# Performance work log

Hardware: AMD Instinct MI355X
Metric: run time of the kernel (lower is better)

## Reference

```python
import jax, jax.numpy as jnp
import numpy as np

N = 100000   # nodes
E = 1600000  # edges (avg degree 16)
D = 64       # input feature dim
H = 64       # hidden dim


def _uniform(k, shape, fan_in):
    s = 1.0 / np.sqrt(fan_in).astype(np.float32)
    return jax.random.uniform(k, shape, jnp.float32, -s, s)


def setup_inputs() -> dict:
    key = jax.random.key(0)
    ks = jax.random.split(key, 9)
    x = jax.random.normal(ks[0], (N, D), jnp.float32)
    edge_index = jax.random.randint(ks[1], (2, E), 0, N, dtype=jnp.int64)
    edge_weight = jax.random.uniform(ks[2], (E,), jnp.float32)
    return {
        "x": x,
        "edge_index": edge_index,
        "edge_weight": edge_weight,
        # conv1: GraphConv(D, H): lin_rel (with bias) + lin_root (no bias)
        "w1_rel": _uniform(ks[3], (H, D), D),
        "b1": _uniform(ks[4], (H,), D),
        "w1_root": _uniform(ks[5], (H, D), D),
        # conv2: GraphConv(H, H)
        "w2_rel": _uniform(ks[6], (H, H), H),
        "b2": _uniform(ks[7], (H,), H),
        "w2_root": _uniform(ks[8], (H, H), H),
    }


def _graph_conv(h, src, dst, ew, w_rel, b, w_root):
    # PyG GraphConv with aggr='add':
    #   out_i = W_rel @ sum_{(j->i) in E} ew_ji * h_j + b + W_root @ h_i
    msg = h[src] * ew[:, None]                              # [E, F] gather
    agg = jax.ops.segment_sum(msg, dst, num_segments=N)     # [N, F] scatter-add
    return agg @ w_rel.T + b + h @ w_root.T


def reference(x, edge_index, edge_weight, w1_rel, b1, w1_root, w2_rel, b2, w2_root):
    src, dst = edge_index[0], edge_index[1]
    # dropout(0.2) is identity in eval mode
    h = jax.nn.relu(_graph_conv(x, src, dst, edge_weight, w1_rel, b1, w1_root))
    h = jax.nn.relu(_graph_conv(h, src, dst, edge_weight, w2_rel, b2, w2_root))
    return h
```

## Files before the change

kernel.cpp:

```cpp
#include <hip/hip_runtime.h>
#include <cstddef>


#define FDIM 64
#define BSHC 9
#define BNC (1 << BSHC)
#define CAPC 8960

static inline size_t align256(size_t x) { return (x + 255) & ~size_t(255); }

typedef __attribute__((ext_vector_type(8))) short bf16x8;
typedef __attribute__((ext_vector_type(4))) float f32x4;

__device__ __forceinline__ ushort f2bf(float f) {
    unsigned u = __float_as_uint(f);
    unsigned r = u + 0x7fffu + ((u >> 16) & 1u);
    return (ushort)(r >> 16);
}
__device__ __forceinline__ float bflo(unsigned g) { return __uint_as_float(g << 16); }
__device__ __forceinline__ float bfhi(unsigned g) { return __uint_as_float(g & 0xffff0000u); }
__device__ __forceinline__ unsigned packbf(float lo, float hi) {
    return (unsigned)f2bf(lo) | ((unsigned)f2bf(hi) << 16);
}

__global__ void __launch_bounds__(256)
k_prep(const float* __restrict__ x, ushort* __restrict__ xb, int nflt,
       const int* __restrict__ ei, int* __restrict__ flag,
       int* __restrict__ gcur, int nbc,
       const float* __restrict__ wrel1, const float* __restrict__ wroot1,
       const float* __restrict__ wrel2, const float* __restrict__ wroot2,
       ushort* __restrict__ wp1, ushort* __restrict__ wp2) {
    int t = threadIdx.x, bid = blockIdx.x;
    int i = (bid * 256 + t) * 4;
    if (i < nflt) {
        float4 v = *reinterpret_cast<const float4*>(x + i);
        ushort4 o;
        o.x = f2bf(v.x); o.y = f2bf(v.y); o.z = f2bf(v.z); o.w = f2bf(v.w);
        *reinterpret_cast<ushort4*>(xb + i) = o;
    }
    if (bid == 0) {
        __shared__ int any;
        if (t == 0) any = 0;
        __syncthreads();
        for (int k = t; k < 2048; k += 256)
            if (ei[2 * k + 1] != 0) any = 1;
        for (int j = t; j < nbc; j += 256) gcur[j] = 0;
        __syncthreads();
        if (t == 0) *flag = (any == 0) ? 1 : 0;
    } else if (bid <= 64) {
        int tid = (bid - 1) * 256 + t;
        int layer = tid >> 13;
        int idx = tid & 8191;
        int j = idx & 7, l = (idx >> 3) & 63, og = (idx >> 9) & 3, kk = idx >> 11;
        int k = kk * 32 + ((l >> 4) << 3) + j;
        int o = og * 16 + (l & 15);
        const float* rel  = layer ? wrel2 : wrel1;
        const float* root = layer ? wroot2 : wroot1;
        float v = (k < 64) ? rel[o * FDIM + k] : root[o * FDIM + (k - 64)];
        (layer ? wp2 : wp1)[idx] = f2bf(v);
    }
}

__global__ void __launch_bounds__(512)
k_scatterC(const int* __restrict__ ei, const float* __restrict__ ew, int E,
           const int* __restrict__ flag, int* __restrict__ gcur,
           uint2* __restrict__ recs, int nbc) {
    __shared__ int hcnt[256];
    __shared__ int hbase[256];
    int t = threadIdx.x;
    int base = blockIdx.x * 4096;
    int sh = *flag;
    if (t < 256) hcnt[t] = 0;
    __syncthreads();

    int bkt[8];
    uint2 rec[8];
#pragma unroll
    for (int j = 0; j < 8; ++j) {
        int e = base + j * 512 + t;
        bkt[j] = -1;
        if (e < E) {
            int s = ei[(size_t)e << sh];
            int d = ei[(size_t)(E + e) << sh];
            bkt[j] = d >> BSHC;
            rec[j].x = (unsigned)s | ((unsigned)(d & (BNC - 1)) << 17);
            rec[j].y = __float_as_uint(ew[e]);
            atomicAdd(&hcnt[bkt[j]], 1);
        }
    }
    __syncthreads();
    if (t < nbc) {
        int c = hcnt[t];
        hbase[t] = c ? (t * CAPC + atomicAdd(&gcur[t], c)) : 0;
    }
    __syncthreads();
    if (t < 256) hcnt[t] = 0;
    __syncthreads();
#pragma unroll
    for (int j = 0; j < 8; ++j) {
        if (bkt[j] >= 0) {
            int r = atomicAdd(&hcnt[bkt[j]], 1);
            int pos = hbase[bkt[j]] + r;
            if (pos < (bkt[j] + 1) * CAPC) recs[pos] = rec[j];
        }
    }
}

__global__ void __launch_bounds__(512)
k_csrSortC(const int* __restrict__ gcur, uint2* __restrict__ recs, int n,
           int* __restrict__ rs, int* __restrict__ re) {
    __shared__ uint2 lrec[CAPC];
    __shared__ int lh[BNC];
    __shared__ int lo[BNC];
    __shared__ int lcur[BNC];
    int b = blockIdx.x, t = threadIdx.x;
    int base = b * CAPC;
    int cnt = gcur[b];
    if (cnt > CAPC) cnt = CAPC;

    for (int i = t; i < cnt; i += 512) lrec[i] = recs[base + i];
    lh[t] = 0;
    __syncthreads();
    for (int i = t; i < cnt; i += 512) atomicAdd(&lh[lrec[i].x >> 17], 1);
    __syncthreads();
    lo[t] = lh[t];
    __syncthreads();
    for (int off = 1; off < BNC; off <<= 1) {
        int v = (t >= off) ? lo[t - off] : 0;
        __syncthreads();
        lo[t] += v;
        __syncthreads();
    }
    {
        int ex = lo[t] - lh[t];
        lcur[t] = ex;
        int node = (b << BSHC) + t;
        if (node < n) { rs[node] = base + ex; re[node] = base + ex + lh[t]; }
    }
    __syncthreads();
    for (int i = t; i < cnt; i += 512) {
        uint2 r = lrec[i];
        int pos = atomicAdd(&lcur[r.x >> 17], 1);
        recs[base + pos] = make_uint2(r.x & 0x1FFFF, r.y);
    }
}

__global__ void __launch_bounds__(256)
k_aggB16(const ushort* __restrict__ hb, const int* __restrict__ rs,
         const int* __restrict__ re, const uint2* __restrict__ recs,
         int n, ushort* __restrict__ aggb) {
    int wavid = (blockIdx.x * blockDim.x + threadIdx.x) >> 6;
    int lane = threadIdx.x & 63;
    int nA = wavid << 1;
    if (nA >= n) return;
    int nB = nA + 1;
    int q = lane >> 3, sl = lane & 7;
    const uint4* hw4 = reinterpret_cast<const uint4*>(hb);
    int pA = rs[nA], eA = re[nA];
    int pB = rs[nB], eB = re[nB];

    float A0 = 0.f, A1 = 0.f, A2 = 0.f, A3 = 0.f, A4 = 0.f, A5 = 0.f, A6 = 0.f, A7 = 0.f;
    float B0 = 0.f, B1 = 0.f, B2 = 0.f, B3 = 0.f, B4 = 0.f, B5 = 0.f, B6 = 0.f, B7 = 0.f;

#define FMA8(P, g, wf)                                       \
    do {                                                     \
        float w_ = (wf);                                     \
        P##0 = fmaf(bflo((g).x), w_, P##0);                  \
        P##1 = fmaf(bfhi((g).x), w_, P##1);                  \
        P##2 = fmaf(bflo((g).y), w_, P##2);                  \
        P##3 = fmaf(bfhi((g).y), w_, P##3);                  \
        P##4 = fmaf(bflo((g).z), w_, P##4);                  \
        P##5 = fmaf(bfhi((g).z), w_, P##5);                  \
        P##6 = fmaf(bflo((g).w), w_, P##6);                  \
        P##7 = fmaf(bfhi((g).w), w_, P##7);                  \
    } while (0)

    while (pA < eA || pB < eB) {
        int iA0 = pA + q, iA1 = pA + 8 + q;
        int iB0 = pB + q, iB1 = pB + 8 + q;
        uint2 ra0 = recs[iA0];
        uint2 ra1 = recs[iA1];
        uint2 rb0 = recs[iB0];
        uint2 rb1 = recs[iB1];
        uint4 ga0 = hw4[(size_t)(ra0.x & 0x1FFFFu) * 8 + sl];
        uint4 ga1 = hw4[(size_t)(ra1.x & 0x1FFFFu) * 8 + sl];
        uint4 gb0 = hw4[(size_t)(rb0.x & 0x1FFFFu) * 8 + sl];
        uint4 gb1 = hw4[(size_t)(rb1.x & 0x1FFFFu) * 8 + sl];
        float wa0 = (iA0 < eA) ? __uint_as_float(ra0.y) : 0.f;
        float wa1 = (iA1 < eA) ? __uint_as_float(ra1.y) : 0.f;
        float wb0 = (iB0 < eB) ? __uint_as_float(rb0.y) : 0.f;
        float wb1 = (iB1 < eB) ? __uint_as_float(rb1.y) : 0.f;
        FMA8(A, ga0, wa0);
        FMA8(A, ga1, wa1);
        FMA8(B, gb0, wb0);
        FMA8(B, gb1, wb1);
        pA = (pA + 16 < eA) ? pA + 16 : eA;
        pB = (pB + 16 < eB) ? pB + 16 : eB;
    }
#undef FMA8

#define RED2(d)                                                  \
    A0 += __shfl_xor(A0, d, 64); A1 += __shfl_xor(A1, d, 64);    \
    A2 += __shfl_xor(A2, d, 64); A3 += __shfl_xor(A3, d, 64);    \
    A4 += __shfl_xor(A4, d, 64); A5 += __shfl_xor(A5, d, 64);    \
    A6 += __shfl_xor(A6, d, 64); A7 += __shfl_xor(A7, d, 64);    \
    B0 += __shfl_xor(B0, d, 64); B1 += __shfl_xor(B1, d, 64);    \
    B2 += __shfl_xor(B2, d, 64); B3 += __shfl_xor(B3, d, 64);    \
    B4 += __shfl_xor(B4, d, 64); B5 += __shfl_xor(B5, d, 64);    \
    B6 += __shfl_xor(B6, d, 64); B7 += __shfl_xor(B7, d, 64);
    RED2(8) RED2(16) RED2(32)
#undef RED2

    if (q == 0) {
        uint4 o;
        o.x = packbf(A0, A1);
        o.y = packbf(A2, A3);
        o.z = packbf(A4, A5);
        o.w = packbf(A6, A7);
        reinterpret_cast<uint4*>(aggb + (size_t)nA * FDIM)[sl] = o;
    } else if (q == 1) {
        uint4 o;
        o.x = packbf(B0, B1);
        o.y = packbf(B2, B3);
        o.z = packbf(B4, B5);
        o.w = packbf(B6, B7);
        reinterpret_cast<uint4*>(aggb + (size_t)nB * FDIM)[sl] = o;
    }
}

template<int OUTBF>
__global__ void __launch_bounds__(256)
k_denseM(const ushort* __restrict__ aggb, const ushort* __restrict__ rootb,
         const ushort* __restrict__ wp, const float* __restrict__ bias,
         float* __restrict__ outp, ushort* __restrict__ outb, int n) {
    int t = threadIdx.x;
    int wv = t >> 6, l = t & 63;
    int n0 = blockIdx.x * 64 + wv * 16;
    int row = l & 15, half = l >> 4;

    int node = n0 + row;
    bool inb = node < n;
    const ushort* ap = aggb + (size_t)node * FDIM + half * 8;
    const ushort* rp = rootb + (size_t)node * FDIM + half * 8;
    bf16x8 a0 = inb ? *reinterpret_cast<const bf16x8*>(ap)      : bf16x8{0,0,0,0,0,0,0,0};
    bf16x8 a1 = inb ? *reinterpret_cast<const bf16x8*>(ap + 32) : bf16x8{0,0,0,0,0,0,0,0};
    bf16x8 a2 = inb ? *reinterpret_cast<const bf16x8*>(rp)      : bf16x8{0,0,0,0,0,0,0,0};
    bf16x8 a3 = inb ? *reinterpret_cast<const bf16x8*>(rp + 32) : bf16x8{0,0,0,0,0,0,0,0};

    f32x4 acc[4];
#pragma unroll
    for (int og = 0; og < 4; ++og) acc[og] = f32x4{0.f, 0.f, 0.f, 0.f};

#pragma unroll
    for (int og = 0; og < 4; ++og) {
        const bf16x8* wb = reinterpret_cast<const bf16x8*>(wp) + og * 64 + l;
        acc[og] = __builtin_amdgcn_mfma_f32_16x16x32_bf16(a0, wb[0],       acc[og], 0, 0, 0);
        acc[og] = __builtin_amdgcn_mfma_f32_16x16x32_bf16(a1, wb[4 * 64],  acc[og], 0, 0, 0);
        acc[og] = __builtin_amdgcn_mfma_f32_16x16x32_bf16(a2, wb[8 * 64],  acc[og], 0, 0, 0);
        acc[og] = __builtin_amdgcn_mfma_f32_16x16x32_bf16(a3, wb[12 * 64], acc[og], 0, 0, 0);
    }

    int rbase = n0 + half * 4;
#pragma unroll
    for (int og = 0; og < 4; ++og) {
        float bb = bias[og * 16 + row];
#pragma unroll
        for (int r = 0; r < 4; ++r) {
            int nd = rbase + r;
            if (nd < n) {
                float v = fmaxf(acc[og][r] + bb, 0.f);
                if (OUTBF) outb[(size_t)nd * FDIM + og * 16 + row] = f2bf(v);
                else       outp[(size_t)nd * FDIM + og * 16 + row] = v;
            }
        }
    }
}

extern "C" void kernel_launch(void* const* d_in, const int* in_sizes, int n_in,
                              void* d_out, int out_size, void* d_ws, size_t ws_size,
                              hipStream_t stream) {
    const float* x      = (const float*)d_in[0];
    const int*   ei     = (const int*)d_in[1];
    const float* ew     = (const float*)d_in[2];
    const float* w1rel  = (const float*)d_in[3];
    const float* b1     = (const float*)d_in[4];
    const float* w1root = (const float*)d_in[5];
    const float* w2rel  = (const float*)d_in[6];
    const float* b2     = (const float*)d_in[7];
    const float* w2root = (const float*)d_in[8];
    float* out = (float*)d_out;

    int N = in_sizes[0] / FDIM;
    int E = in_sizes[2];
    int NBC = (N + BNC - 1) >> BSHC;

    char* w = (char*)d_ws;
    int* flag    = (int*)w;    w += align256(256);
    int* gcur    = (int*)w;    w += align256((size_t)NBC * 4);
    int* rs      = (int*)w;    w += align256((size_t)N * 4);
    int* re      = (int*)w;    w += align256((size_t)N * 4);
    ushort* wp1  = (ushort*)w; w += align256(8192 * 2);
    ushort* wp2  = (ushort*)w; w += align256(8192 * 2);
    uint2* recs  = (uint2*)w;  w += align256((size_t)NBC * CAPC * 8);
    ushort* aggb = (ushort*)w; w += align256((size_t)N * FDIM * 2);
    ushort* xb   = (ushort*)w; w += align256((size_t)N * FDIM * 2);
    ushort* h1b  = (ushort*)w; w += align256((size_t)N * FDIM * 2);

    int nflt = N * FDIM;
    k_prep<<<(nflt / 4 + 255) / 256, 256, 0, stream>>>(
        x, xb, nflt, ei, flag, gcur, NBC, w1rel, w1root, w2rel, w2root, wp1, wp2);
    k_scatterC<<<(E + 4095) / 4096, 512, 0, stream>>>(ei, ew, E, flag, gcur, recs, NBC);
    k_csrSortC<<<NBC, 512, 0, stream>>>(gcur, recs, N, rs, re);

    k_aggB16<<<(N + 7) / 8, 256, 0, stream>>>(xb, rs, re, recs, N, aggb);
    k_denseM<1><<<(N + 63) / 64, 256, 0, stream>>>(aggb, xb, wp1, b1, nullptr, h1b, N);
    k_aggB16<<<(N + 7) / 8, 256, 0, stream>>>(h1b, rs, re, recs, N, aggb);
    k_denseM<0><<<(N + 63) / 64, 256, 0, stream>>>(aggb, h1b, wp2, b2, out, nullptr, N);
}
```

Baseline: 140.7 us.

## Rework aggregation: half-wave per node, shuffle-broadcast edge records, adaptive gather depth

The aggregation kernel now assigns each half-wave to one node. The half-wave loads up to 32 edge records at once with one coalesced load, then broadcasts the source indices and weights through shuffles. Up to 8 gather steps are issued per iteration, limited by the remaining degree, so low-degree nodes do not fetch wasted rows. A zeroed 64-entry pad is placed after the record buffer so that reads past the end stay safe. The cross-lane reduction drops one shuffle stage, at the cost of more shuffle traffic per edge and wave-uniform control flow.

```diff
diff --git a/kernel.cpp b/kernel.cpp
--- a/kernel.cpp
+++ b/kernel.cpp
@@ -26,7 +26,7 @@
 __global__ void __launch_bounds__(256)
 k_prep(const float* __restrict__ x, ushort* __restrict__ xb, int nflt,
        const int* __restrict__ ei, int* __restrict__ flag,
-       int* __restrict__ gcur, int nbc,
+       int* __restrict__ gcur, int nbc, uint2* __restrict__ pad,
        const float* __restrict__ wrel1, const float* __restrict__ wroot1,
        const float* __restrict__ wrel2, const float* __restrict__ wroot2,
        ushort* __restrict__ wp1, ushort* __restrict__ wp2) {
@@ -45,6 +45,7 @@
         for (int k = t; k < 2048; k += 256)
             if (ei[2 * k + 1] != 0) any = 1;
         for (int j = t; j < nbc; j += 256) gcur[j] = 0;
+        if (t < 64) pad[t] = make_uint2(0u, 0u);
         __syncthreads();
         if (t == 0) *flag = (any == 0) ? 1 : 0;
     } else if (bid <= 64) {
@@ -153,78 +154,84 @@
     int lane = threadIdx.x & 63;
     int nA = wavid << 1;
     if (nA >= n) return;
-    int nB = nA + 1;
-    int q = lane >> 3, sl = lane & 7;
+    int half = lane >> 5;
+    int r2 = (lane >> 3) & 3;
+    int sl = lane & 7;
+    int node = nA + half;
+    int p = rs[node], e = re[node];
     const uint4* hw4 = reinterpret_cast<const uint4*>(hb);
-    int pA = rs[nA], eA = re[nA];
-    int pB = rs[nB], eB = re[nB];
-
-    float A0 = 0.f, A1 = 0.f, A2 = 0.f, A3 = 0.f, A4 = 0.f, A5 = 0.f, A6 = 0.f, A7 = 0.f;
-    float B0 = 0.f, B1 = 0.f, B2 = 0.f, B3 = 0.f, B4 = 0.f, B5 = 0.f, B6 = 0.f, B7 = 0.f;
-
-#define FMA8(P, g, wf)                                       \
-    do {                                                     \
-        float w_ = (wf);                                     \
-        P##0 = fmaf(bflo((g).x), w_, P##0);                  \
-        P##1 = fmaf(bfhi((g).x), w_, P##1);                  \
-        P##2 = fmaf(bflo((g).y), w_, P##2);                  \
-        P##3 = fmaf(bfhi((g).y), w_, P##3);                  \
-        P##4 = fmaf(bflo((g).z), w_, P##4);                  \
-        P##5 = fmaf(bfhi((g).z), w_, P##5);                  \
-        P##6 = fmaf(bflo((g).w), w_, P##6);                  \
-        P##7 = fmaf(bfhi((g).w), w_, P##7);                  \
+
+    float a0 = 0.f, a1 = 0.f, a2 = 0.f, a3 = 0.f;
+    float a4 = 0.f, a5 = 0.f, a6 = 0.f, a7 = 0.f;
+
+#define FMA8(g, wf)                                        \
+    do {                                                   \
+        float w_ = (wf);                                   \
+        a0 = fmaf(bflo((g).x), w_, a0);                    \
+        a1 = fmaf(bfhi((g).x), w_, a1);                    \
+        a2 = fmaf(bflo((g).y), w_, a2);                    \
+        a3 = fmaf(bfhi((g).y), w_, a3);                    \
+        a4 = fmaf(bflo((g).z), w_, a4);                    \
+        a5 = fmaf(bfhi((g).z), w_, a5);                    \
+        a6 = fmaf(bflo((g).w), w_, a6);                    \
+        a7 = fmaf(bfhi((g).w), w_, a7);                    \
     } while (0)
 
-    while (pA < eA || pB < eB) {
-        int iA0 = pA + q, iA1 = pA + 8 + q;
-        int iB0 = pB + q, iB1 = pB + 8 + q;
-        uint2 ra0 = recs[iA0];
-        uint2 ra1 = recs[iA1];
-        uint2 rb0 = recs[iB0];
-        uint2 rb1 = recs[iB1];
-        uint4 ga0 = hw4[(size_t)(ra0.x & 0x1FFFFu) * 8 + sl];
-        uint4 ga1 = hw4[(size_t)(ra1.x & 0x1FFFFu) * 8 + sl];
-        uint4 gb0 = hw4[(size_t)(rb0.x & 0x1FFFFu) * 8 + sl];
-        uint4 gb1 = hw4[(size_t)(rb1.x & 0x1FFFFu) * 8 + sl];
-        float wa0 = (iA0 < eA) ? __uint_as_float(ra0.y) : 0.f;
-        float wa1 = (iA1 < eA) ? __uint_as_float(ra1.y) : 0.f;
-        float wb0 = (iB0 < eB) ? __uint_as_float(rb0.y) : 0.f;
-        float wb1 = (iB1 < eB) ? __uint_as_float(rb1.y) : 0.f;
-        FMA8(A, ga0, wa0);
-        FMA8(A, ga1, wa1);
-        FMA8(B, gb0, wb0);
-        FMA8(B, gb1, wb1);
-        pA = (pA + 16 < eA) ? pA + 16 : eA;
-        pB = (pB + 16 < eB) ? pB + 16 : eB;
+    while (__any(p < e)) {
+        uint2 rc = recs[p + (lane & 31)];
+        int rem = e - p;
+        int vmax = max(rem, __shfl_xor(rem, 32, 64));
+        int gmax = (vmax + 3) >> 2;
+        if (gmax > 8) gmax = 8;
+
+#define GSTEP(G, GV, WV)                                           \
+        uint4 GV = {0u, 0u, 0u, 0u}; float WV = 0.f;               \
+        if (G < gmax) {                                            \
+            int off_ = (G << 2) + r2;                              \
+            int srl_ = (half << 5) + off_;                         \
+            unsigned sx_ = __shfl(rc.x, srl_, 64);                 \
+            unsigned sw_ = __shfl(rc.y, srl_, 64);                 \
+            GV = hw4[(size_t)(sx_ & 0x1FFFFu) * 8 + sl];           \
+            WV = (off_ < rem) ? __uint_as_float(sw_) : 0.f;        \
+        }
+        GSTEP(0, gv0, w0)
+        GSTEP(1, gv1, w1)
+        GSTEP(2, gv2, w2)
+        GSTEP(3, gv3, w3)
+        GSTEP(4, gv4, w4)
+        GSTEP(5, gv5, w5)
+        GSTEP(6, gv6, w6)
+        GSTEP(7, gv7, w7)
+#undef GSTEP
+
+        FMA8(gv0, w0);
+        if (1 < gmax) FMA8(gv1, w1);
+        if (2 < gmax) FMA8(gv2, w2);
+        if (3 < gmax) FMA8(gv3, w3);
+        if (4 < gmax) FMA8(gv4, w4);
+        if (5 < gmax) FMA8(gv5, w5);
+        if (6 < gmax) FMA8(gv6, w6);
+        if (7 < gmax) FMA8(gv7, w7);
+
+        p = (p + 32 < e) ? p + 32 : e;
     }
 #undef FMA8
 
-#define RED2(d)                                                  \
-    A0 += __shfl_xor(A0, d, 64); A1 += __shfl_xor(A1, d, 64);    \
-    A2 += __shfl_xor(A2, d, 64); A3 += __shfl_xor(A3, d, 64);    \
-    A4 += __shfl_xor(A4, d, 64); A5 += __shfl_xor(A5, d, 64);    \
-    A6 += __shfl_xor(A6, d, 64); A7 += __shfl_xor(A7, d, 64);    \
-    B0 += __shfl_xor(B0, d, 64); B1 += __shfl_xor(B1, d, 64);    \
-    B2 += __shfl_xor(B2, d, 64); B3 += __shfl_xor(B3, d, 64);    \
-    B4 += __shfl_xor(B4, d, 64); B5 += __shfl_xor(B5, d, 64);    \
-    B6 += __shfl_xor(B6, d, 64); B7 += __shfl_xor(B7, d, 64);
-    RED2(8) RED2(16) RED2(32)
-#undef RED2
-
-    if (q == 0) {
+#define RED(d)                                                 \
+    a0 += __shfl_xor(a0, d, 64); a1 += __shfl_xor(a1, d, 64);  \
+    a2 += __shfl_xor(a2, d, 64); a3 += __shfl_xor(a3, d, 64);  \
+    a4 += __shfl_xor(a4, d, 64); a5 += __shfl_xor(a5, d, 64);  \
+    a6 += __shfl_xor(a6, d, 64); a7 += __shfl_xor(a7, d, 64);
+    RED(8) RED(16)
+#undef RED
+
+    if (r2 == 0) {
         uint4 o;
-        o.x = packbf(A0, A1);
-        o.y = packbf(A2, A3);
-        o.z = packbf(A4, A5);
-        o.w = packbf(A6, A7);
-        reinterpret_cast<uint4*>(aggb + (size_t)nA * FDIM)[sl] = o;
-    } else if (q == 1) {
-        uint4 o;
-        o.x = packbf(B0, B1);
-        o.y = packbf(B2, B3);
-        o.z = packbf(B4, B5);
-        o.w = packbf(B6, B7);
-        reinterpret_cast<uint4*>(aggb + (size_t)nB * FDIM)[sl] = o;
+        o.x = packbf(a0, a1);
+        o.y = packbf(a2, a3);
+        o.z = packbf(a4, a5);
+        o.w = packbf(a6, a7);
+        reinterpret_cast<uint4*>(aggb + (size_t)node * FDIM)[sl] = o;
     }
 }
 
@@ -301,14 +308,15 @@
     int* re      = (int*)w;    w += align256((size_t)N * 4);
     ushort* wp1  = (ushort*)w; w += align256(8192 * 2);
     ushort* wp2  = (ushort*)w; w += align256(8192 * 2);
-    uint2* recs  = (uint2*)w;  w += align256((size_t)NBC * CAPC * 8);
+    uint2* recs  = (uint2*)w;  w += align256(((size_t)NBC * CAPC + 64) * 8);
     ushort* aggb = (ushort*)w; w += align256((size_t)N * FDIM * 2);
     ushort* xb   = (ushort*)w; w += align256((size_t)N * FDIM * 2);
     ushort* h1b  = (ushort*)w; w += align256((size_t)N * FDIM * 2);
 
     int nflt = N * FDIM;
     k_prep<<<(nflt / 4 + 255) / 256, 256, 0, stream>>>(
-        x, xb, nflt, ei, flag, gcur, NBC, w1rel, w1root, w2rel, w2root, wp1, wp2);
+        x, xb, nflt, ei, flag, gcur, NBC, recs + (size_t)NBC * CAPC,
+        w1rel, w1root, w2rel, w2root, wp1, wp2);
     k_scatterC<<<(E + 4095) / 4096, 512, 0, stream>>>(ei, ew, E, flag, gcur, recs, NBC);
     k_csrSortC<<<NBC, 512, 0, stream>>>(gcur, recs, N, rs, re);
 
```

After: 150.3 us. 1.07x slower.

## Fuse prep and edge-bucket scatter into one kernel with role-split blocks

Applied to the files above, without the earlier changes.

Merges the prep kernel (x to bf16 conversion, weight packing, int64-layout detection, counter reset) and the edge scatter kernel into a single launch. Blocks are partitioned by index into scatter, weight-pack and conversion roles. Each scatter block now detects the index layout itself instead of reading a flag, and the counter reset becomes a memset. This removes one kernel launch and the dependency between the two stages so they can overlap. In exchange, every scatter block repeats the 2048-entry layout probe and an extra memset node is added.

```diff
diff --git a/kernel.cpp b/kernel.cpp
--- a/kernel.cpp
+++ b/kernel.cpp
@@ -23,32 +23,29 @@
     return (unsigned)f2bf(lo) | ((unsigned)f2bf(hi) << 16);
 }
 
-__global__ void __launch_bounds__(256)
-k_prep(const float* __restrict__ x, ushort* __restrict__ xb, int nflt,
-       const int* __restrict__ ei, int* __restrict__ flag,
-       int* __restrict__ gcur, int nbc,
-       const float* __restrict__ wrel1, const float* __restrict__ wroot1,
-       const float* __restrict__ wrel2, const float* __restrict__ wroot2,
-       ushort* __restrict__ wp1, ushort* __restrict__ wp2) {
+__global__ void __launch_bounds__(512)
+k_fused(const int* __restrict__ ei, const float* __restrict__ ew, int E,
+        int* __restrict__ gcur, uint2* __restrict__ recs, int nbc, int sb,
+        const float* __restrict__ x, ushort* __restrict__ xb, int nflt,
+        const float* __restrict__ wrel1, const float* __restrict__ wroot1,
+        const float* __restrict__ wrel2, const float* __restrict__ wroot2,
+        ushort* __restrict__ wp1, ushort* __restrict__ wp2, int nbf) {
     int t = threadIdx.x, bid = blockIdx.x;
-    int i = (bid * 256 + t) * 4;
-    if (i < nflt) {
-        float4 v = *reinterpret_cast<const float4*>(x + i);
-        ushort4 o;
-        o.x = f2bf(v.x); o.y = f2bf(v.y); o.z = f2bf(v.z); o.w = f2bf(v.w);
-        *reinterpret_cast<ushort4*>(xb + i) = o;
-    }
-    if (bid == 0) {
-        __shared__ int any;
-        if (t == 0) any = 0;
-        __syncthreads();
-        for (int k = t; k < 2048; k += 256)
-            if (ei[2 * k + 1] != 0) any = 1;
-        for (int j = t; j < nbc; j += 256) gcur[j] = 0;
-        __syncthreads();
-        if (t == 0) *flag = (any == 0) ? 1 : 0;
-    } else if (bid <= 64) {
-        int tid = (bid - 1) * 256 + t;
+
+    if (bid >= sb + 32) {
+        int stride = nbf * 512;
+        int nq = nflt >> 2;
+        for (int iq = (bid - sb - 32) * 512 + t; iq < nq; iq += stride) {
+            int i = iq * 4;
+            float4 v = *reinterpret_cast<const float4*>(x + i);
+            ushort4 o;
+            o.x = f2bf(v.x); o.y = f2bf(v.y); o.z = f2bf(v.z); o.w = f2bf(v.w);
+            *reinterpret_cast<ushort4*>(xb + i) = o;
+        }
+        return;
+    }
+    if (bid >= sb) {
+        int tid = (bid - sb) * 512 + t;
         int layer = tid >> 13;
         int idx = tid & 8191;
         int j = idx & 7, l = (idx >> 3) & 63, og = (idx >> 9) & 3, kk = idx >> 11;
@@ -58,21 +55,21 @@
         const float* root = layer ? wroot2 : wroot1;
         float v = (k < 64) ? rel[o * FDIM + k] : root[o * FDIM + (k - 64)];
         (layer ? wp2 : wp1)[idx] = f2bf(v);
-    }
-}
-
-__global__ void __launch_bounds__(512)
-k_scatterC(const int* __restrict__ ei, const float* __restrict__ ew, int E,
-           const int* __restrict__ flag, int* __restrict__ gcur,
-           uint2* __restrict__ recs, int nbc) {
+        return;
+    }
+
+    __shared__ int any;
     __shared__ int hcnt[256];
     __shared__ int hbase[256];
-    int t = threadIdx.x;
-    int base = blockIdx.x * 4096;
-    int sh = *flag;
+    if (t == 0) any = 0;
     if (t < 256) hcnt[t] = 0;
     __syncthreads();
-
+    for (int k = t; k < 2048; k += 512)
+        if (ei[2 * k + 1] != 0) any = 1;
+    __syncthreads();
+    int sh = (any == 0) ? 1 : 0;
+
+    int base = bid * 4096;
     int bkt[8];
     uint2 rec[8];
 #pragma unroll
@@ -293,23 +290,25 @@
     int N = in_sizes[0] / FDIM;
     int E = in_sizes[2];
     int NBC = (N + BNC - 1) >> BSHC;
+    int SB  = (E + 4095) / 4096;
+    int NBF = 782;
 
     char* w = (char*)d_ws;
-    int* flag    = (int*)w;    w += align256(256);
     int* gcur    = (int*)w;    w += align256((size_t)NBC * 4);
     int* rs      = (int*)w;    w += align256((size_t)N * 4);
     int* re      = (int*)w;    w += align256((size_t)N * 4);
     ushort* wp1  = (ushort*)w; w += align256(8192 * 2);
     ushort* wp2  = (ushort*)w; w += align256(8192 * 2);
-    uint2* recs  = (uint2*)w;  w += align256((size_t)NBC * CAPC * 8);
+    uint2* recs  = (uint2*)w;  w += align256(((size_t)NBC * CAPC + 64) * 8);
     ushort* aggb = (ushort*)w; w += align256((size_t)N * FDIM * 2);
     ushort* xb   = (ushort*)w; w += align256((size_t)N * FDIM * 2);
     ushort* h1b  = (ushort*)w; w += align256((size_t)N * FDIM * 2);
 
     int nflt = N * FDIM;
-    k_prep<<<(nflt / 4 + 255) / 256, 256, 0, stream>>>(
-        x, xb, nflt, ei, flag, gcur, NBC, w1rel, w1root, w2rel, w2root, wp1, wp2);
-    k_scatterC<<<(E + 4095) / 4096, 512, 0, stream>>>(ei, ew, E, flag, gcur, recs, NBC);
+    hipMemsetAsync(gcur, 0, (size_t)NBC * sizeof(int), stream);
+    k_fused<<<SB + 32 + NBF, 512, 0, stream>>>(
+        ei, ew, E, gcur, recs, NBC, SB, x, xb, nflt,
+        w1rel, w1root, w2rel, w2root, wp1, wp2, NBF);
     k_csrSortC<<<NBC, 512, 0, stream>>>(gcur, recs, N, rs, re);
 
     k_aggB16<<<(N + 7) / 8, 256, 0, stream>>>(xb, rs, re, recs, N, aggb);
```

Result: no change. 142.3 us (+1.2%).
